# Performance work log

Hardware: AMD Instinct MI355X
Metric: run time of the kernel (lower is better)

## Reference

```python
import jax, jax.numpy as jnp
import numpy as np

N = 100000   # num_nodes
E = 1600000  # num_edges
R = 8        # num_rels
B = 4        # num_bases
D = 64       # inp_dim = h_dim = out_dim


def setup_inputs() -> dict:
    key = jax.random.key(0)
    ks = jax.random.split(key, 16)
    s = 1.0 / np.sqrt(D)
    inp = {
        'h': jax.random.normal(ks[0], (N, D), jnp.float32),
        'src': jax.random.randint(ks[1], (E,), 0, N),
        'dst': jax.random.randint(ks[2], (E,), 0, N),
        'etype': jax.random.randint(ks[3], (E,), 0, R),
        'norm': jax.random.uniform(ks[4], (E, 1), jnp.float32),
    }
    for i in range(3):  # i2h, hidden, h2o layers (basis decomposition)
        inp[f'bases{i}'] = jax.random.normal(ks[5 + 2 * i], (B, D, D), jnp.float32) * s
        inp[f'wcomp{i}'] = jax.random.normal(ks[6 + 2 * i], (R, B), jnp.float32) * s
    inp['dec_w1'] = jax.random.normal(ks[11], (D, D), jnp.float32) * s
    inp['dec_b1'] = jnp.zeros((D,), jnp.float32)
    inp['dec_w2'] = jax.random.normal(ks[12], (D, 1), jnp.float32) * s
    inp['dec_b2'] = jnp.zeros((1,), jnp.float32)
    return inp


def rgcn_layer(h, src, dst, etype, norm, bases, wcomp, activate):
    # basis decomposition: W_r = sum_b wcomp[r,b] * bases[b]
    W = jnp.einsum('rb,bio->rio', wcomp, bases)           # [R, D, D]
    # transform all nodes under every relation (dense GEMM), then gather per edge
    Ht = jnp.einsum('ni,rio->rno', h, W).reshape(R * N, -1)  # [R*N, D]
    msg = Ht[etype * N + src] * norm                      # [E, D] gather + norm
    out = jax.ops.segment_sum(msg, dst, num_segments=N)   # scatter-add to dst
    return jax.nn.relu(out) if activate else out


def reference(h, src, dst, etype, norm, bases0, wcomp0, bases1, wcomp1,
              bases2, wcomp2, dec_w1, dec_b1, dec_w2, dec_b2):
    # EncoderRGCN: i2h (relu) -> hidden (relu) -> h2o (no activation)
    h1 = rgcn_layer(h, src, dst, etype, norm, bases0, wcomp0, True)
    h2 = rgcn_layer(h1, src, dst, etype, norm, bases1, wcomp1, True)
    henc = rgcn_layer(h2, src, dst, etype, norm, bases2, wcomp2, False)
    # AttributeDecoder: Linear -> ReLU -> Linear(reconstruct_dim=1)
    d1 = jax.nn.relu(henc @ dec_w1 + dec_b1)
    rec = (d1 @ dec_w2 + dec_b2).squeeze()                # [N]
    return rec, henc
```

## Files before the change

kernel.cpp:

```cpp
#include <hip/hip_runtime.h>

typedef _Float16 half8 __attribute__((ext_vector_type(8)));
typedef _Float16 half4 __attribute__((ext_vector_type(4)));
typedef _Float16 half2v __attribute__((ext_vector_type(2)));
typedef float floatx4 __attribute__((ext_vector_type(4)));

constexpr int NN = 100000;
constexpr int EE = 1600000;
constexpr int NBK = 391;
constexpr int CHUNK = 3125;
constexpr int CAPB = 6144;
constexpr int NDCAP = 48;

__global__ __launch_bounds__(512) void k_part(const int* __restrict__ dst,
                                              const int* __restrict__ src,
                                              const int* __restrict__ etype,
                                              const float* __restrict__ norm,
                                              int* __restrict__ gcur,
                                              int2* __restrict__ part) {
  __shared__ int2 ldata[CHUNK];
  __shared__ unsigned short lbkt[CHUNK];
  __shared__ int lhist[NBK], lbase[NBK + 1], lcur[NBK], gbase[NBK];
  __shared__ int swsum[8];
  const int tid = threadIdx.x;
  const int e0 = blockIdx.x * CHUNK;

  if (tid < NBK) lhist[tid] = 0;
  __syncthreads();
  for (int i = tid; i < CHUNK; i += 512)
    atomicAdd(&lhist[dst[e0 + i] >> 8], 1);
  __syncthreads();
  {
    const int v = (tid < NBK) ? lhist[tid] : 0;
    int incl = v;
    for (int d = 1; d < 64; d <<= 1) {
      const int t = __shfl_up(incl, d);
      if ((tid & 63) >= d) incl += t;
    }
    if ((tid & 63) == 63) swsum[tid >> 6] = incl;
    __syncthreads();
    int pre = 0;
    for (int w = 0; w < (tid >> 6); ++w) pre += swsum[w];
    const int excl = pre + incl - v;
    if (tid < NBK) {
      lbase[tid] = excl;
      lcur[tid] = 0;
      gbase[tid] = tid * CAPB + atomicAdd(&gcur[tid], v);
    }
    if (tid == 0) lbase[NBK] = CHUNK;
  }
  __syncthreads();
  for (int i = tid; i < CHUNK; i += 512) {
    const int e = e0 + i;
    const int d = dst[e], s = src[e], et = etype[e];
    const _Float16 nh = (_Float16)norm[e];
    const unsigned short n16 = __builtin_bit_cast(unsigned short, nh);
    const int bk = d >> 8;
    const int pos = lbase[bk] + atomicAdd(&lcur[bk], 1);
    ldata[pos] = make_int2((d << 15) | (s >> 2), (s & 3) | (et << 2) | ((int)n16 << 5));
    lbkt[pos] = (unsigned short)bk;
  }
  __syncthreads();
  for (int i = tid; i < CHUNK; i += 512) {
    const int bk = (int)lbkt[i];
    part[gbase[bk] + (i - lbase[bk])] = ldata[i];
  }
}

__global__ __launch_bounds__(1024) void k_part2(const int* __restrict__ gcur,
                                                const int2* __restrict__ part,
                                                int* __restrict__ off,
                                                int2* __restrict__ em) {
  __shared__ int hcnt[256];
  __shared__ int wred[16];
  __shared__ int swsum[4];
  const int tid = threadIdx.x;
  const int bk = blockIdx.x;
  const int nb0 = bk << 8;
  const int2* __restrict__ pp = part + (size_t)bk * CAPB;

  {
    int pv = (tid < bk) ? gcur[tid] : 0;
    for (int d = 32; d > 0; d >>= 1) pv += __shfl_down(pv, d);
    if ((tid & 63) == 0) wred[tid >> 6] = pv;
  }
  if (tid < 256) hcnt[tid] = 0;
  __syncthreads();
  int base = 0;
#pragma unroll
  for (int w = 0; w < 16; ++w) base += wred[w];
  const int cntb = gcur[bk];

  for (int i = tid; i < cntb; i += 1024)
    atomicAdd(&hcnt[(((unsigned)pp[i].x) >> 15) & 255], 1);
  __syncthreads();
  const int v = (tid < 256) ? hcnt[tid] : 0;
  int incl = v;
  for (int d = 1; d < 64; d <<= 1) {
    const int t = __shfl_up(incl, d);
    if ((tid & 63) >= d) incl += t;
  }
  if (tid < 256 && (tid & 63) == 63) swsum[tid >> 6] = incl;
  __syncthreads();
  if (tid < 256) {
    int pre = 0;
    for (int w = 0; w < (tid >> 6); ++w) pre += swsum[w];
    const int excl = pre + incl - v;
    const int n = nb0 + tid;
    if (n < NN) off[n] = base + excl;
    hcnt[tid] = excl;
  }
  if (bk == NBK - 1 && tid == 0) off[NN] = EE;
  __syncthreads();
  for (int i = tid; i < cntb; i += 1024) {
    const int2 r = pp[i];
    const int d = ((unsigned)r.x) >> 15;
    const int s = ((r.x & 0x7FFF) << 2) | (r.y & 3);
    const int et = (r.y >> 2) & 7;
    const unsigned short n16 = (unsigned short)((r.y >> 5) & 0xFFFF);
    const float nf = (float)__builtin_bit_cast(_Float16, n16);
    const int pos = atomicAdd(&hcnt[d & 255], 1);
    em[base + pos] = make_int2(((d & 15) << 23) | (et << 20) | s, __float_as_int(nf));
  }
}


__global__ __launch_bounds__(256) void k_prep(const float* __restrict__ h,
                                              _Float16* __restrict__ hh,
                                              const float* __restrict__ b0,
                                              const float* __restrict__ b1,
                                              const float* __restrict__ b2,
                                              _Float16* __restrict__ bbt,
                                              int* __restrict__ gcur) {
  const int bx = blockIdx.x;
  if (bx == 0) {
    for (int i = threadIdx.x; i < NBK; i += 256) gcur[i] = 0;
  }
  if (bx < 6250) {
    const int i = bx * 256 + threadIdx.x;
    const float4 v = *(const float4*)&h[(size_t)i * 4];
    half4 o = {(_Float16)v.x, (_Float16)v.y, (_Float16)v.z, (_Float16)v.w};
    *(half4*)&hh[(size_t)i * 4] = o;
  } else {
    const int g = (bx - 6250) >> 6;
    const int idx = ((bx - 6250) & 63) * 256 + threadIdx.x;
    const float* bases = (g == 0) ? b0 : (g == 1) ? b1 : b2;
    const int o = idx >> 8, k = idx & 255;
    const int b = k >> 6, i = k & 63;
    bbt[g * 16384 + idx] = (_Float16)bases[b * 4096 + i * 64 + o];
  }
}

__global__ __launch_bounds__(256, 8) void k_layer(const _Float16* __restrict__ hh,
                                                  const int* __restrict__ off,
                                                  const int2* __restrict__ em,
                                                  const float* __restrict__ wcomp,
                                                  const _Float16* __restrict__ bbt,
                                                  _Float16* __restrict__ out16,
                                                  float* __restrict__ out32) {
  __shared__ _Float16 Ash[16 * 264];
  __shared__ int  ems_s[16 * NDCAP];
  __shared__ int2 ems_c[16 * NDCAP];
  __shared__ float4 wcs[8];
  __shared__ int offs[17];
  __shared__ int ovf;
  const int tid = threadIdx.x;
  const int lane = tid & 63;
  const int wv = tid >> 6;
  const int n0 = blockIdx.x * 16;

  if (tid < 17) offs[tid] = off[n0 + tid];
  if (tid == 0) ovf = 0;
  if (tid < 8) wcs[tid] = ((const float4*)wcomp)[tid];
  {
    const int4 z4 = make_int4(0, 0, 0, 0);
    int4* zs = (int4*)ems_s;
    int4* zc = (int4*)ems_c;
    if (tid < 192) zs[tid] = z4;
    for (int i = tid; i < 384; i += 256) zc[i] = z4;
  }
  __syncthreads();

  const int e0 = offs[0];
  const int len = offs[16] - e0;
  for (int i = tid; i < len; i += 256) {
    const int g = e0 + i;
    const int2 r = em[g];
    const int lo = (r.x >> 23) & 15;
    const int rank = g - offs[lo];
    const int et = (r.x >> 20) & 7;
    const int s = r.x & 0xFFFFF;
    const float nf = __int_as_float(r.y);
    const float4 w = wcs[et];
    const _Float16 c0 = (_Float16)(nf * w.x), c1 = (_Float16)(nf * w.y);
    const _Float16 c2 = (_Float16)(nf * w.z), c3 = (_Float16)(nf * w.w);
    const half2v p01 = {c0, c1}, p23 = {c2, c3};
    if (rank < NDCAP) {
      ems_s[lo * NDCAP + rank] = s;
      ems_c[lo * NDCAP + rank] = make_int2(
          __builtin_bit_cast(int, p01), __builtin_bit_cast(int, p23));
    } else ovf = 1;
  }
  __syncthreads();

#define LOADB(mm, bb, hv)                                                      \
  {                                                                            \
    const int4* sp4_ = (const int4*)&ems_s[(mm) * NDCAP + (bb) * 16 + eg * 8]; \
    const int4 sa_ = sp4_[0], sb_ = sp4_[1];                                   \
    hv[0] = hp[(unsigned)sa_.x * 32u + fl];                                    \
    hv[1] = hp[(unsigned)sa_.y * 32u + fl];                                    \
    hv[2] = hp[(unsigned)sa_.z * 32u + fl];                                    \
    hv[3] = hp[(unsigned)sa_.w * 32u + fl];                                    \
    hv[4] = hp[(unsigned)sb_.x * 32u + fl];                                    \
    hv[5] = hp[(unsigned)sb_.y * 32u + fl];                                    \
    hv[6] = hp[(unsigned)sb_.z * 32u + fl];                                    \
    hv[7] = hp[(unsigned)sb_.w * 32u + fl];                                    \
  }

#define FMAQ(mm, bb, hv, aq)                                                   \
  {                                                                            \
    const int4* cp4_ = (const int4*)&ems_c[(mm) * NDCAP + (bb) * 16 + eg * 8]; \
    _Pragma("unroll")                                                          \
    for (int k_ = 0; k_ < 4; ++k_) {                                           \
      const int4 c_ = cp4_[k_];                                                \
      const half2v pa01_ = __builtin_bit_cast(half2v, c_.x);                   \
      const half2v pa23_ = __builtin_bit_cast(half2v, c_.y);                   \
      const half2v pb01_ = __builtin_bit_cast(half2v, c_.z);                   \
      const half2v pb23_ = __builtin_bit_cast(half2v, c_.w);                   \
      aq[0] = aq[0] + hv[2 * k_] * __builtin_shufflevector(pa01_, pa01_, 0, 0);\
      aq[1] = aq[1] + hv[2 * k_] * __builtin_shufflevector(pa01_, pa01_, 1, 1);\
      aq[2] = aq[2] + hv[2 * k_] * __builtin_shufflevector(pa23_, pa23_, 0, 0);\
      aq[3] = aq[3] + hv[2 * k_] * __builtin_shufflevector(pa23_, pa23_, 1, 1);\
      aq[0] = aq[0] + hv[2 * k_ + 1] * __builtin_shufflevector(pb01_, pb01_, 0, 0);\
      aq[1] = aq[1] + hv[2 * k_ + 1] * __builtin_shufflevector(pb01_, pb01_, 1, 1);\
      aq[2] = aq[2] + hv[2 * k_ + 1] * __builtin_shufflevector(pb23_, pb23_, 0, 0);\
      aq[3] = aq[3] + hv[2 * k_ + 1] * __builtin_shufflevector(pb23_, pb23_, 1, 1);\
    }                                                                          \
  }

  if (!ovf) {
    const int fl = lane & 31;
    const int eg = lane >> 5;
    const half2v* __restrict__ hp = (const half2v*)hh;
    const int mb = wv * 4;
    const int oA = offs[mb], oB = offs[mb + 1], oC = offs[mb + 2],
              oD = offs[mb + 3], oE = offs[mb + 4];
    const int c0n = oB - oA, c1n = oC - oB, c2n = oD - oC, c3n = oE - oD;
    const int nb0_ = (c0n > 0) ? ((c0n + 15) >> 4) : 1;
    const int nb1_ = (c1n > 0) ? ((c1n + 15) >> 4) : 1;
    const int nb2_ = (c2n > 0) ? ((c2n + 15) >> 4) : 1;
    const int nb3_ = (c3n > 0) ? ((c3n + 15) >> 4) : 1;

    half2v acc[4][4];
#pragma unroll
    for (int q = 0; q < 4; ++q)
#pragma unroll
      for (int i = 0; i < 4; ++i) acc[q][i] = half2v{0, 0};

    half2v hvA[8], hvB[8];
    LOADB(mb, 0, hvA);
#pragma unroll
    for (int q = 0; q < 4; ++q) {
      const int m = mb + q;
      const int nbq = (q == 0) ? nb0_ : (q == 1) ? nb1_ : (q == 2) ? nb2_ : nb3_;
      if (q < 3) {
        if (q & 1) LOADB(m + 1, 0, hvA) else LOADB(m + 1, 0, hvB)
      }
      if (q & 1) FMAQ(m, 0, hvB, acc[q]) else FMAQ(m, 0, hvA, acc[q])
      for (int b = 1; b < nbq; ++b) {
        if (q & 1) {
          LOADB(m, b, hvB) FMAQ(m, b, hvB, acc[q])
        } else {
          LOADB(m, b, hvA) FMAQ(m, b, hvA, acc[q])
        }
      }
    }
#pragma unroll
    for (int q = 0; q < 4; ++q) {
      const int m = mb + q;
#pragma unroll
      for (int i = 0; i < 4; ++i)
        acc[q][i] = acc[q][i] + __builtin_bit_cast(half2v,
            __shfl_xor(__builtin_bit_cast(int, acc[q][i]), 32));
      if (eg == 0) {
        _Float16* ar = &Ash[m * 264];
        *(half2v*)&ar[0 * 64 + 2 * fl] = acc[q][0];
        *(half2v*)&ar[1 * 64 + 2 * fl] = acc[q][1];
        *(half2v*)&ar[2 * 64 + 2 * fl] = acc[q][2];
        *(half2v*)&ar[3 * 64 + 2 * fl] = acc[q][3];
      }
    }
  } else {
    const _Float16* hl = hh + lane;
    for (int q = 0; q < 4; ++q) {
      const int m = wv * 4 + q;
      const int p0 = offs[m], p1 = offs[m + 1];
      float a0 = 0.f, a1 = 0.f, a2 = 0.f, a3 = 0.f;
      for (int p = p0; p < p1; p += 8) {
#pragma unroll
        for (int j = 0; j < 8; ++j) {
          const bool live = (p + j < p1);
          const int idx = live ? p + j : p1 - 1;
          const int2 mm = em[idx];
          const float hv = (float)hl[(size_t)(mm.x & 0xFFFFF) << 6];
          const float wn = live ? __int_as_float(mm.y) : 0.f;
          const float4 w = wcs[(mm.x >> 20) & 7];
          const float t = wn * hv;
          a0 = fmaf(t, w.x, a0); a1 = fmaf(t, w.y, a1);
          a2 = fmaf(t, w.z, a2); a3 = fmaf(t, w.w, a3);
        }
      }
      _Float16* ar = &Ash[m * 264];
      ar[lane]       = (_Float16)a0;
      ar[64 + lane]  = (_Float16)a1;
      ar[128 + lane] = (_Float16)a2;
      ar[192 + lane] = (_Float16)a3;
    }
  }
  __syncthreads();

  const int col = lane & 15;
  const int quad = lane >> 4;
  const int obase = wv * 16 + col;
  const _Float16* ap = &Ash[col * 264 + quad * 8];
  const _Float16* bp = &bbt[(size_t)obase * 256 + quad * 8];
  floatx4 acc2 = {0.f, 0.f, 0.f, 0.f};
#pragma unroll
  for (int s = 0; s < 8; ++s) {
    const half8 af = *(const half8*)(ap + s * 32);
    const half8 bf = *(const half8*)(bp + s * 32);
    acc2 = __builtin_amdgcn_mfma_f32_16x16x32_f16(af, bf, acc2, 0, 0, 0);
  }
  if (out16) {
#pragma unroll
    for (int r = 0; r < 4; ++r) {
      const float c = fmaxf(acc2[r], 0.f);
      out16[(size_t)(n0 + quad * 4 + r) * 64 + obase] = (_Float16)c;
    }
  } else {
#pragma unroll
    for (int r = 0; r < 4; ++r) {
      out32[(size_t)(n0 + quad * 4 + r) * 64 + obase] = acc2[r];
    }
  }
#undef LOADB
#undef FMAQ
}

__global__ __launch_bounds__(256) void k_dec(const float* __restrict__ henc,
                                             const float* __restrict__ w1,
                                             const float* __restrict__ b1,
                                             const float* __restrict__ w2,
                                             const float* __restrict__ b2,
                                             float* __restrict__ rec) {
  __shared__ float w1s[64 * 64];
  __shared__ float hs[16 * 68];
  const int tid = threadIdx.x;
  for (int r = tid; r < 1024; r += 256)
    *(float4*)&w1s[r * 4] = *(const float4*)&w1[r * 4];
  const int og = tid & 15;
  const int nl = tid >> 4;
  const float4 wv2 = *(const float4*)&w2[og * 4];
  const float4 bv1 = *(const float4*)&b1[og * 4];
  const float b2v = b2[0];
  for (int t0 = blockIdx.x * 16; t0 < NN; t0 += gridDim.x * 16) {
    __syncthreads();
    {
      const float4 hv = *(const float4*)&henc[(size_t)t0 * 64 + tid * 4];
      *(float4*)&hs[(tid >> 4) * 68 + (tid & 15) * 4] = hv;
    }
    __syncthreads();
    float4 acc = bv1;
    const float* hr = &hs[nl * 68];
#pragma unroll 8
    for (int i = 0; i < 64; ++i) {
      const float hv = hr[i];
      const float4 wv = *(const float4*)&w1s[i * 64 + og * 4];
      acc.x = fmaf(hv, wv.x, acc.x); acc.y = fmaf(hv, wv.y, acc.y);
      acc.z = fmaf(hv, wv.z, acc.z); acc.w = fmaf(hv, wv.w, acc.w);
    }
    acc.x = fmaxf(acc.x, 0.f); acc.y = fmaxf(acc.y, 0.f);
    acc.z = fmaxf(acc.z, 0.f); acc.w = fmaxf(acc.w, 0.f);
    float v = acc.x * wv2.x + acc.y * wv2.y + acc.z * wv2.z + acc.w * wv2.w;
    v += __shfl_xor(v, 1); v += __shfl_xor(v, 2);
    v += __shfl_xor(v, 4); v += __shfl_xor(v, 8);
    if (og == 0) rec[t0 + nl] = v + b2v;
  }
}


extern "C" void kernel_launch(void* const* d_in, const int* in_sizes, int n_in,
                              void* d_out, int out_size, void* d_ws, size_t ws_size,
                              hipStream_t stream) {
  const float* h     = (const float*)d_in[0];
  const int*   src   = (const int*)d_in[1];
  const int*   dst   = (const int*)d_in[2];
  const int*   etype = (const int*)d_in[3];
  const float* norm  = (const float*)d_in[4];
  const float* bases[3] = {(const float*)d_in[5], (const float*)d_in[7], (const float*)d_in[9]};
  const float* wcomp[3] = {(const float*)d_in[6], (const float*)d_in[8], (const float*)d_in[10]};
  const float* dw1 = (const float*)d_in[11];
  const float* db1 = (const float*)d_in[12];
  const float* dw2 = (const float*)d_in[13];
  const float* db2 = (const float*)d_in[14];

  float* rec  = (float*)d_out;
  float* henc = (float*)d_out + NN;

  char* ws = (char*)d_ws;
  int*      off    = (int*)(ws + 0);
  int*      gcur   = (int*)(ws + 400512);
  int2*     em     = (int2*)(ws + 402560);
  _Float16* hh     = (_Float16*)(ws + 13202560);
  _Float16* h1f    = (_Float16*)(ws + 26002560);
  _Float16* h2f    = (_Float16*)(ws + 38802560);
  _Float16* bbt    = (_Float16*)(ws + 51602560);
  int2*     part   = (int2*)h1f;

  k_prep<<<6250 + 192, 256, 0, stream>>>(h, hh, bases[0], bases[1], bases[2], bbt, gcur);

  k_part<<<512, 512, 0, stream>>>(dst, src, etype, norm, gcur, part);
  k_part2<<<NBK, 1024, 0, stream>>>(gcur, part, off, em);

  k_layer<<<NN / 16, 256, 0, stream>>>(hh,  off, em, wcomp[0], bbt,         h1f, nullptr);
  k_layer<<<NN / 16, 256, 0, stream>>>(h1f, off, em, wcomp[1], bbt + 16384, h2f, nullptr);
  k_layer<<<NN / 16, 256, 0, stream>>>(h2f, off, em, wcomp[2], bbt + 32768, nullptr, henc);

  k_dec<<<1024, 256, 0, stream>>>(henc, dw1, db1, dw2, db2, rec);
}
```

Before: 321.0 us.

## Fuse prep into partition kernel, cache bucket records in LDS, use packed fp16 convert

Merges the fp16 conversion of h and bases into the partition kernel as extra blocks and zeroes gcur with a memset, which removes one kernel launch and lets the two jobs run concurrently. The second partition pass now stages bucket records in shared memory so they are read from global memory once instead of twice, with a fallback when a bucket exceeds LDS capacity. Coefficient packing uses the cvt_pkrtz intrinsic, which rounds toward zero instead of to nearest. The cost is slight precision drift and larger per-block LDS in k_part2, which may lower occupancy.

New measurement: 318.1 us, median of 2. No clear change (-0.9%).

```diff
diff --git a/kernel.cpp b/kernel.cpp
--- a/kernel.cpp
+++ b/kernel.cpp
@@ -10,20 +10,47 @@
 constexpr int NBK = 391;
 constexpr int CHUNK = 3125;
 constexpr int CAPB = 6144;
+constexpr int LCAP = 4608;
 constexpr int NDCAP = 48;
 
-__global__ __launch_bounds__(512) void k_part(const int* __restrict__ dst,
-                                              const int* __restrict__ src,
-                                              const int* __restrict__ etype,
-                                              const float* __restrict__ norm,
-                                              int* __restrict__ gcur,
-                                              int2* __restrict__ part) {
+__global__ __launch_bounds__(512) void k_partprep(const int* __restrict__ dst,
+                                                  const int* __restrict__ src,
+                                                  const int* __restrict__ etype,
+                                                  const float* __restrict__ norm,
+                                                  int* __restrict__ gcur,
+                                                  int2* __restrict__ part,
+                                                  const float* __restrict__ h,
+                                                  _Float16* __restrict__ hh,
+                                                  const float* __restrict__ b0,
+                                                  const float* __restrict__ b1,
+                                                  const float* __restrict__ b2,
+                                                  _Float16* __restrict__ bbt) {
   __shared__ int2 ldata[CHUNK];
   __shared__ unsigned short lbkt[CHUNK];
   __shared__ int lhist[NBK], lbase[NBK + 1], lcur[NBK], gbase[NBK];
   __shared__ int swsum[8];
   const int tid = threadIdx.x;
-  const int e0 = blockIdx.x * CHUNK;
+  const int bx = blockIdx.x;
+
+  if (bx >= 512) {
+    if (bx < 3637) {
+      const int i = (bx - 512) * 512 + tid;
+      const float4 v = *(const float4*)&h[(size_t)i * 4];
+      half4 o = {(_Float16)v.x, (_Float16)v.y, (_Float16)v.z, (_Float16)v.w};
+      *(half4*)&hh[(size_t)i * 4] = o;
+    } else {
+      const int L = (bx - 3637) * 512 + tid;
+      const int g = L >> 14;
+      const int idx = L & 16383;
+      const float* bases = (g == 0) ? b0 : (g == 1) ? b1 : b2;
+      const int o = idx >> 8, k = idx & 255;
+      const int b = k >> 6, i = k & 63;
+      bbt[g * 16384 + idx] = (_Float16)bases[b * 4096 + i * 64 + o];
+    }
+    return;
+  }
+
+  const int e0 = bx * CHUNK;
 
   if (tid < NBK) lhist[tid] = 0;
   __syncthreads();
@@ -71,6 +98,7 @@
                                                 const int2* __restrict__ part,
                                                 int* __restrict__ off,
                                                 int2* __restrict__ em) {
+  __shared__ int2 lrec[LCAP];
   __shared__ int hcnt[256];
   __shared__ int wred[16];
   __shared__ int swsum[4];
@@ -90,9 +118,18 @@
 #pragma unroll
   for (int w = 0; w < 16; ++w) base += wred[w];
   const int cntb = gcur[bk];
-
-  for (int i = tid; i < cntb; i += 1024)
-    atomicAdd(&hcnt[(((unsigned)pp[i].x) >> 15) & 255], 1);
+  const bool uselds = (cntb <= LCAP);
+
+  if (uselds) {
+    for (int i = tid; i < cntb; i += 1024) {
+      const int2 r = pp[i];
+      lrec[i] = r;
+      atomicAdd(&hcnt[(((unsigned)r.x) >> 15) & 255], 1);
+    }
+  } else {
+    for (int i = tid; i < cntb; i += 1024)
+      atomicAdd(&hcnt[(((unsigned)pp[i].x) >> 15) & 255], 1);
+  }
   __syncthreads();
   const int v = (tid < 256) ? hcnt[tid] : 0;
   int incl = v;
@@ -113,7 +150,7 @@
   if (bk == NBK - 1 && tid == 0) off[NN] = EE;
   __syncthreads();
   for (int i = tid; i < cntb; i += 1024) {
-    const int2 r = pp[i];
+    const int2 r = uselds ? lrec[i] : pp[i];
     const int d = ((unsigned)r.x) >> 15;
     const int s = ((r.x & 0x7FFF) << 2) | (r.y & 3);
     const int et = (r.y >> 2) & 7;
@@ -121,33 +158,6 @@
     const float nf = (float)__builtin_bit_cast(_Float16, n16);
     const int pos = atomicAdd(&hcnt[d & 255], 1);
     em[base + pos] = make_int2(((d & 15) << 23) | (et << 20) | s, __float_as_int(nf));
-  }
-}
-
-
-__global__ __launch_bounds__(256) void k_prep(const float* __restrict__ h,
-                                              _Float16* __restrict__ hh,
-                                              const float* __restrict__ b0,
-                                              const float* __restrict__ b1,
-                                              const float* __restrict__ b2,
-                                              _Float16* __restrict__ bbt,
-                                              int* __restrict__ gcur) {
-  const int bx = blockIdx.x;
-  if (bx == 0) {
-    for (int i = threadIdx.x; i < NBK; i += 256) gcur[i] = 0;
-  }
-  if (bx < 6250) {
-    const int i = bx * 256 + threadIdx.x;
-    const float4 v = *(const float4*)&h[(size_t)i * 4];
-    half4 o = {(_Float16)v.x, (_Float16)v.y, (_Float16)v.z, (_Float16)v.w};
-    *(half4*)&hh[(size_t)i * 4] = o;
-  } else {
-    const int g = (bx - 6250) >> 6;
-    const int idx = ((bx - 6250) & 63) * 256 + threadIdx.x;
-    const float* bases = (g == 0) ? b0 : (g == 1) ? b1 : b2;
-    const int o = idx >> 8, k = idx & 255;
-    const int b = k >> 6, i = k & 63;
-    bbt[g * 16384 + idx] = (_Float16)bases[b * 4096 + i * 64 + o];
   }
 }
 
@@ -192,13 +202,11 @@
     const int s = r.x & 0xFFFFF;
     const float nf = __int_as_float(r.y);
     const float4 w = wcs[et];
-    const _Float16 c0 = (_Float16)(nf * w.x), c1 = (_Float16)(nf * w.y);
-    const _Float16 c2 = (_Float16)(nf * w.z), c3 = (_Float16)(nf * w.w);
-    const half2v p01 = {c0, c1}, p23 = {c2, c3};
+    const int p01i = __builtin_bit_cast(int, __builtin_amdgcn_cvt_pkrtz(nf * w.x, nf * w.y));
+    const int p23i = __builtin_bit_cast(int, __builtin_amdgcn_cvt_pkrtz(nf * w.z, nf * w.w));
     if (rank < NDCAP) {
       ems_s[lo * NDCAP + rank] = s;
-      ems_c[lo * NDCAP + rank] = make_int2(
-          __builtin_bit_cast(int, p01), __builtin_bit_cast(int, p23));
+      ems_c[lo * NDCAP + rank] = make_int2(p01i, p23i);
     } else ovf = 1;
   }
   __syncthreads();
@@ -417,9 +425,10 @@
   _Float16* bbt    = (_Float16*)(ws + 51602560);
   int2*     part   = (int2*)h1f;
 
-  k_prep<<<6250 + 192, 256, 0, stream>>>(h, hh, bases[0], bases[1], bases[2], bbt, gcur);
-
-  k_part<<<512, 512, 0, stream>>>(dst, src, etype, norm, gcur, part);
+  hipMemsetAsync(gcur, 0, NBK * sizeof(int), stream);
+
+  k_partprep<<<3733, 512, 0, stream>>>(dst, src, etype, norm, gcur, part,
+                                       h, hh, bases[0], bases[1], bases[2], bbt);
   k_part2<<<NBK, 1024, 0, stream>>>(gcur, part, off, em);
 
   k_layer<<<NN / 16, 256, 0, stream>>>(hh,  off, em, wcomp[0], bbt,         h1f, nullptr);
```
